# Kernel optimization log

Hardware: AMD Instinct MI355X
Metric: run time of the kernel (lower is better)

## Reference

```python
import jax, jax.numpy as jnp
import numpy as np

L_LANDMARKS = 64


def hyp_dist(x, y, c):
    """Faithful port of _compute_hyperbolic_distance for 3-D x,y.
    x:(B,N,D), y:(B,M,D) -> (B,N,M). Note: sqrt_c is computed but unused in the
    original, so only c enters via the `factor` term."""
    xn = jnp.sum(x * x, axis=-1)            # (B,N)
    yn = jnp.sum(y * y, axis=-1)            # (B,M)
    diff_sq = xn[:, :, None] + yn[:, None, :] - 2.0 * jnp.einsum('bnd,bmd->bnm', x, y)
    diff_sq = jnp.maximum(diff_sq, 1e-10)
    factor = (1.0 + c * xn)[:, :, None] + c * yn[:, None, :]
    return jnp.sqrt(diff_sq) * jnp.sqrt(jnp.maximum(factor, 1e-6))


def select_landmarks(emb, L, c):
    """MaxMin landmark selection. Original seeds with torch.randint; we use a
    deterministic seed index 0 per batch for reproducibility."""
    B, N, D = emb.shape
    first = jnp.zeros((B,), jnp.int32)

    def step(carry, _):
        min_d, prev = carry
        lm = jnp.take_along_axis(emb, prev[:, None, None].astype(jnp.int32), axis=1)  # (B,1,D)
        d = hyp_dist(emb, lm, c)[:, :, 0]        # (B,N)
        min_d = jnp.minimum(min_d, d)
        nxt = jnp.argmax(min_d, axis=1).astype(jnp.int32)
        return (min_d, nxt), nxt

    init = (jnp.full((B, N), jnp.inf, emb.dtype), first)
    _, rest = jax.lax.scan(step, init, None, length=L - 1)   # (L-1, B)
    idx = jnp.concatenate([first[None, :], rest], axis=0).T   # (B, L)
    landmarks = jnp.take_along_axis(emb, idx[:, :, None], axis=1)  # (B,L,D)
    return landmarks, idx


def witness_edge_weights(emb, landmarks, c):
    """Vectorized witness complex: for every point take its 2 nearest landmarks
    (i,j) and scatter-min the witness distance (dist to 2nd nearest) into the
    symmetric (L,L) edge weight matrix. Replaces the original B*N python loop."""
    B, N, D = emb.shape
    L = landmarks.shape[1]
    d = hyp_dist(emb, landmarks, c)              # (B,N,L)
    neg, idx2 = jax.lax.top_k(-d, 2)             # 2 smallest distances
    wd = -neg[..., 1]                            # witness distance (B,N)
    i = jnp.minimum(idx2[..., 0], idx2[..., 1])
    j = jnp.maximum(idx2[..., 0], idx2[..., 1])
    ew = jnp.full((B, L, L), jnp.inf, d.dtype)
    b = jnp.broadcast_to(jnp.arange(B)[:, None], (B, N))
    ew = ew.at[b, i, j].min(wd)
    ew = jnp.minimum(ew, jnp.swapaxes(ew, 1, 2))  # symmetrize
    return ew


def connected_components(adj):
    """Min-label propagation over the boolean adjacency; converges in <= L
    steps. labels[i] == min node index in i's component."""
    B, L, _ = adj.shape
    labels = jnp.broadcast_to(jnp.arange(L), (B, L))

    def body(_, labels):
        nb = jnp.min(jnp.where(adj, labels[:, None, :], L), axis=2)  # (B,L)
        return jnp.minimum(labels, nb)

    labels = jax.lax.fori_loop(0, L, body, labels)
    return jnp.sum(labels == jnp.arange(L), axis=1)  # number of components


def setup_inputs() -> dict:
    key = jax.random.key(0)
    k1, _ = jax.random.split(key)
    embeddings = jax.random.normal(k1, (8, 16384, 256), dtype=jnp.float32)
    curvature_scale = jnp.ones((), dtype=jnp.float32)
    return {"embeddings": embeddings, "curvature_scale": curvature_scale}


def reference(embeddings, curvature_scale):
    B, N, D = embeddings.shape
    L = min(L_LANDMARKS, N)
    c = jnp.abs(curvature_scale)
    landmarks, _ = select_landmarks(embeddings, L, c)
    ew = witness_edge_weights(embeddings, landmarks, c)
    adj = jnp.isfinite(ew)                       # (B,L,L), diag stays inf
    ncomp = connected_components(adj)            # (B,)
    n_edges = jnp.sum(jnp.triu(adj.astype(jnp.int32), 1), axis=(1, 2))
    # Kruskal-style counting: each redundant (cycle-closing) edge is a loop.
    beta_0 = ncomp.astype(jnp.float32)
    beta_1 = (n_edges - (L - ncomp)).astype(jnp.float32)
    fragmentation_score = beta_0 / L
    circular_reasoning = beta_1 > 3.0            # threshold_beta1 = 3
    return (beta_0, beta_1, fragmentation_score, circular_reasoning)
```

## Files before the change

### kernel.cpp

```cpp
#include <hip/hip_runtime.h>

static constexpr int B_ = 8;
static constexpr int N_ = 16384;
static constexpr int D_ = 256;
static constexpr int L_ = 64;

static constexpr int TPB = 512;
static constexpr int LF4 = 18;
static constexpr int RF4 = 64 - LF4;


__global__ void __launch_bounds__(1024)
init_kernel(unsigned int* __restrict__ z)
{
    z[blockIdx.x * 1024 + threadIdx.x] = 0u;
}

__global__ __attribute__((amdgpu_flat_work_group_size(512, 512),
                          amdgpu_waves_per_eu(2, 2)))
void fps_all_kernel(const float* __restrict__ emb, const float* __restrict__ csp,
                    unsigned long long* __restrict__ rec,
                    unsigned int* __restrict__ gadj,
                    unsigned int* __restrict__ cnt,
                    float* __restrict__ out)
{
    const int wg  = blockIdx.x;
    const int b   = wg & 7;
    const int wib = wg >> 3;
    const int tid = threadIdx.x;
    const int n   = (wib << 9) + tid;
    const float c = fabsf(csp[0]);

    __shared__ float4 slab[LF4 * TPB];
    __shared__ float wval[8];
    __shared__ int   widx[8];
    __shared__ float wxn[8];
    __shared__ int   s_next;
    __shared__ float s_lmn;
    __shared__ int   s_lead;
    __shared__ unsigned int lmask[128];
    __shared__ int   labels[64];

    if (tid < 128) lmask[tid] = 0u;

    const float4* __restrict__ pt = (const float4*)(emb + (size_t)(b * N_ + n) * D_);

    float4 p[RF4];
    float s0 = 0.f, s1 = 0.f, s2 = 0.f, s3 = 0.f;
    #pragma unroll
    for (int k = 0; k < LF4; ++k) {
        float4 v = pt[k];
        slab[k * TPB + tid] = v;
        s0 = fmaf(v.x, v.x, s0); s1 = fmaf(v.y, v.y, s1);
        s2 = fmaf(v.z, v.z, s2); s3 = fmaf(v.w, v.w, s3);
    }
    #pragma unroll
    for (int k = 0; k < RF4; ++k) {
        float4 v = pt[LF4 + k];
        p[k] = v;
        s0 = fmaf(v.x, v.x, s0); s1 = fmaf(v.y, v.y, s1);
        s2 = fmaf(v.z, v.z, s2); s3 = fmaf(v.w, v.w, s3);
    }
    const float my_xn = (s0 + s1) + (s2 + s3);

    float min_d = __builtin_inff();
    float b1v = __builtin_inff(), b2v = __builtin_inff();
    int   b1i = 0, b2i = 0;
    int   lm    = 0;
    float lmn_c = 0.f;

    #pragma unroll 1
    for (int s = 1; s <= L_; ++s) {
        const int lmU = __builtin_amdgcn_readfirstlane(lm);
        const float4* __restrict__ w4 =
            (const float4*)(emb + (size_t)(b * N_ + lmU) * D_);

        float lmn;
        if (s == 1) {
            float t0 = 0.f, t1 = 0.f, t2 = 0.f, t3 = 0.f;
            #pragma unroll
            for (int k = 0; k < 64; ++k) {
                float4 w = w4[k];
                t0 = fmaf(w.x, w.x, t0); t1 = fmaf(w.y, w.y, t1);
                t2 = fmaf(w.z, w.z, t2); t3 = fmaf(w.w, w.w, t3);
            }
            lmn = (t0 + t1) + (t2 + t3);
        } else {
            lmn = lmn_c;
        }

        float d0 = 0.f, d1 = 0.f, d2 = 0.f, d3 = 0.f;
        #pragma unroll
        for (int k = 0; k < LF4; ++k) {
            float4 v = slab[k * TPB + tid];
            float4 w = w4[k];
            d0 = fmaf(v.x, w.x, d0); d1 = fmaf(v.y, w.y, d1);
            d2 = fmaf(v.z, w.z, d2); d3 = fmaf(v.w, w.w, d3);
        }
        #pragma unroll
        for (int k = 0; k < RF4; ++k) {
            float4 v = p[k];
            float4 w = w4[LF4 + k];
            d0 = fmaf(v.x, w.x, d0); d1 = fmaf(v.y, w.y, d1);
            d2 = fmaf(v.z, w.z, d2); d3 = fmaf(v.w, w.w, d3);
        }
        const float dot  = (d0 + d1) + (d2 + d3);
        const float diff = fmaxf(my_xn + lmn - 2.f * dot, 1e-10f);
        const float fac  = fmaxf(1.f + c * my_xn + c * lmn, 1e-6f);
        const float d    = sqrtf(diff) * sqrtf(fac);

        if (d < b1v)      { b2v = b1v; b2i = b1i; b1v = d; b1i = s - 1; }
        else if (d < b2v) { b2v = d; b2i = s - 1; }

        if (s == L_) break;

        min_d = fminf(min_d, d);

        float v = min_d; int i = n; float x = my_xn;
        #pragma unroll
        for (int off = 32; off >= 1; off >>= 1) {
            float ov = __shfl_down(v, off);
            int   oi = __shfl_down(i, off);
            float ox = __shfl_down(x, off);
            if (ov > v || (ov == v && oi < i)) { v = ov; i = oi; x = ox; }
        }
        if ((tid & 63) == 0) {
            const int w = tid >> 6;
            wval[w] = v; widx[w] = i; wxn[w] = x;
        }
        __syncthreads();

        if (tid < 64) {
            v = (tid < 8) ? wval[tid] : -__builtin_inff();
            i = (tid < 8) ? widx[tid] : 0x7FFFFFFF;
            x = (tid < 8) ? wxn[tid]  : 0.f;
            #pragma unroll
            for (int off = 4; off >= 1; off >>= 1) {
                float ov = __shfl_down(v, off);
                int   oi = __shfl_down(i, off);
                float ox = __shfl_down(x, off);
                if (ov > v || (ov == v && oi < i)) { v = ov; i = oi; x = ox; }
            }
            const size_t sbase = (size_t)(b * 2 + (s & 1)) * 32 * 16;
            if (tid == 0) {
                const unsigned long long key =
                    ((unsigned long long)__float_as_uint(v) << 32) |
                    ((unsigned)(s & 0xFF) << 14) |
                    (unsigned)(16383 - i);
                const unsigned long long enc64 =
                    ((unsigned long long)(unsigned)s << 32) |
                    (unsigned long long)(unsigned)__float_as_uint(x);
                __hip_atomic_store(&rec[sbase + (size_t)wib * 16 + 0], key,
                                   __ATOMIC_RELAXED, __HIP_MEMORY_SCOPE_AGENT);
                __hip_atomic_store(&rec[sbase + (size_t)wib * 16 + 1], enc64,
                                   __ATOMIC_RELAXED, __HIP_MEMORY_SCOPE_AGENT);
            }
            unsigned long long myk, mye;
            for (;;) {
                myk = __hip_atomic_load(&rec[sbase + (size_t)(tid & 31) * 16 + 0],
                                        __ATOMIC_RELAXED, __HIP_MEMORY_SCOPE_AGENT);
                mye = __hip_atomic_load(&rec[sbase + (size_t)(tid & 31) * 16 + 1],
                                        __ATOMIC_RELAXED, __HIP_MEMORY_SCOPE_AGENT);
                const bool ok = (((myk >> 14) & 0xFFull) == (unsigned long long)(s & 0xFF)) &&
                                ((mye >> 32) == (unsigned long long)(unsigned)s);
                if (__all(ok)) break;
            }
            unsigned long long k = myk, e = mye;
            #pragma unroll
            for (int off = 32; off >= 1; off >>= 1) {
                unsigned long long ok2 = __shfl_down(k, off);
                unsigned long long oe  = __shfl_down(e, off);
                if (ok2 > k) { k = ok2; e = oe; }
            }
            if (tid == 0) {
                s_next = (int)(16383u - (unsigned)(k & 0x3FFFull));
                s_lmn  = __uint_as_float((unsigned)(e & 0xFFFFFFFFull));
            }
        }
        __syncthreads();
        lm    = s_next;
        lmn_c = s_lmn;
    }

    {
        const int lo = min(b1i, b2i), hi = max(b1i, b2i);
        const int bitpos = lo * 64 + hi;
        atomicOr(&lmask[bitpos >> 5], 1u << (bitpos & 31));
    }
    __syncthreads();
    if (tid < 128) {
        unsigned w = lmask[tid];
        if (w) atomicOr(&gadj[b * 128 + tid], w);
    }
    __syncthreads();

    if (tid == 0) {
        __threadfence();
        unsigned prev = atomicAdd(&cnt[b], 1u);
        s_lead = (prev == 31u) ? 1 : 0;
    }
    __syncthreads();
    if (!s_lead) return;

    __threadfence();
    if (tid < 128) lmask[tid] = atomicOr(&gadj[b * 128 + tid], 0u);
    __syncthreads();

    unsigned long long m = 0ull;
    if (tid < 64) {
        m = ((unsigned long long)lmask[tid * 2 + 1] << 32) | lmask[tid * 2];
        for (int j = 0; j < 64; ++j)
            if (lmask[j * 2 + (tid >> 5)] & (1u << (tid & 31))) m |= 1ull << j;
        labels[tid] = tid;
    }
    __syncthreads();

    for (int it = 0; it < 64; ++it) {
        int mn = 0;
        if (tid < 64) {
            mn = labels[tid];
            unsigned long long mm = m;
            while (mm) {
                int j = __ffsll(mm) - 1;
                int lj = labels[j];
                mn = mn < lj ? mn : lj;
                mm &= mm - 1;
            }
        }
        __syncthreads();
        if (tid < 64) labels[tid] = mn;
        __syncthreads();
    }

    if (tid < 64) {
        unsigned long long hi_mask = (tid < 63) ? (~0ull << (tid + 1)) : 0ull;
        int myedges = __popcll(m & hi_mask);
        int mycomp  = (labels[tid] == tid) ? 1 : 0;
        #pragma unroll
        for (int off = 32; off >= 1; off >>= 1) {
            myedges += __shfl_down(myedges, off);
            mycomp  += __shfl_down(mycomp, off);
        }
        if (tid == 0) {
            float beta0 = (float)mycomp;
            float beta1 = (float)(myedges - (64 - mycomp));
            out[b]      = beta0;
            out[8 + b]  = beta1;
            out[16 + b] = beta0 / 64.f;
            out[24 + b] = (beta1 > 3.f) ? 1.f : 0.f;
        }
    }
}

extern "C" void kernel_launch(void* const* d_in, const int* in_sizes, int n_in,
                              void* d_out, int out_size, void* d_ws, size_t ws_size,
                              hipStream_t stream)
{
    const float* emb = (const float*)d_in[0];
    const float* cs  = (const float*)d_in[1];
    float* out = (float*)d_out;

    char* ws = (char*)d_ws;
    unsigned long long* rec  = (unsigned long long*)(ws);
    unsigned int*       gadj = (unsigned int*)(ws + 65536);
    unsigned int*       cnt  = (unsigned int*)(ws + 69632);

    hipLaunchKernelGGL(init_kernel, dim3(18), dim3(1024), 0, stream,
                       (unsigned int*)ws);
    hipLaunchKernelGGL(fps_all_kernel, dim3(256), dim3(TPB), 0, stream,
                       emb, cs, rec, gadj, cnt, out);
}
```

Before: 554.2 us.

## Use leader-based reduce-and-broadcast for per-step cross-workgroup argmax

Replaces the all-to-all exchange, where each of the 32 workgroups per batch polled all 32 records, with a two-phase scheme. Records are packed contiguously. Workgroup 0 polls them, reduces to the global argmax and broadcasts the result into per-workgroup padded slots, and the other workgroups poll only their own slot. The goal is less polling traffic and cache-line contention on the global barrier. The cost is an extra serialized hop through the leader on every one of the 64 steps.

```diff
diff --git a/kernel.cpp b/kernel.cpp
--- a/kernel.cpp
+++ b/kernel.cpp
@@ -20,6 +20,7 @@
                           amdgpu_waves_per_eu(2, 2)))
 void fps_all_kernel(const float* __restrict__ emb, const float* __restrict__ csp,
                     unsigned long long* __restrict__ rec,
+                    unsigned long long* __restrict__ bcast,
                     unsigned int* __restrict__ gadj,
                     unsigned int* __restrict__ cnt,
                     float* __restrict__ out)
@@ -130,6 +131,12 @@
         }
         __syncthreads();
 
+        const int par = s & 1;
+        const size_t recbase = (size_t)(b * 2 + par) * 64;
+        const size_t bbase   = (size_t)(b * 2 + par) * 32 * 16;
+        const unsigned long long tagk = (unsigned long long)(s & 0xFF);
+        const unsigned long long tage = (unsigned long long)(unsigned)s;
+
         if (tid < 64) {
             v = (tid < 8) ? wval[tid] : -__builtin_inff();
             i = (tid < 8) ? widx[tid] : 0x7FFFFFFF;
@@ -141,7 +148,6 @@
                 float ox = __shfl_down(x, off);
                 if (ov > v || (ov == v && oi < i)) { v = ov; i = oi; x = ox; }
             }
-            const size_t sbase = (size_t)(b * 2 + (s & 1)) * 32 * 16;
             if (tid == 0) {
                 const unsigned long long key =
                     ((unsigned long long)__float_as_uint(v) << 32) |
@@ -150,31 +156,54 @@
                 const unsigned long long enc64 =
                     ((unsigned long long)(unsigned)s << 32) |
                     (unsigned long long)(unsigned)__float_as_uint(x);
-                __hip_atomic_store(&rec[sbase + (size_t)wib * 16 + 0], key,
+                __hip_atomic_store(&rec[recbase + (size_t)wib * 2 + 0], key,
                                    __ATOMIC_RELAXED, __HIP_MEMORY_SCOPE_AGENT);
-                __hip_atomic_store(&rec[sbase + (size_t)wib * 16 + 1], enc64,
+                __hip_atomic_store(&rec[recbase + (size_t)wib * 2 + 1], enc64,
                                    __ATOMIC_RELAXED, __HIP_MEMORY_SCOPE_AGENT);
             }
-            unsigned long long myk, mye;
-            for (;;) {
-                myk = __hip_atomic_load(&rec[sbase + (size_t)(tid & 31) * 16 + 0],
-                                        __ATOMIC_RELAXED, __HIP_MEMORY_SCOPE_AGENT);
-                mye = __hip_atomic_load(&rec[sbase + (size_t)(tid & 31) * 16 + 1],
-                                        __ATOMIC_RELAXED, __HIP_MEMORY_SCOPE_AGENT);
-                const bool ok = (((myk >> 14) & 0xFFull) == (unsigned long long)(s & 0xFF)) &&
-                                ((mye >> 32) == (unsigned long long)(unsigned)s);
-                if (__all(ok)) break;
-            }
-            unsigned long long k = myk, e = mye;
-            #pragma unroll
-            for (int off = 32; off >= 1; off >>= 1) {
-                unsigned long long ok2 = __shfl_down(k, off);
-                unsigned long long oe  = __shfl_down(e, off);
-                if (ok2 > k) { k = ok2; e = oe; }
-            }
-            if (tid == 0) {
-                s_next = (int)(16383u - (unsigned)(k & 0x3FFFull));
-                s_lmn  = __uint_as_float((unsigned)(e & 0xFFFFFFFFull));
+
+            if (wib == 0) {
+                unsigned long long myw;
+                for (;;) {
+                    myw = __hip_atomic_load(&rec[recbase + tid],
+                                            __ATOMIC_RELAXED, __HIP_MEMORY_SCOPE_AGENT);
+                    const bool ok = ((tid & 1) == 0)
+                        ? (((myw >> 14) & 0xFFull) == tagk)
+                        : ((myw >> 32) == tage);
+                    if (__all(ok)) break;
+                }
+                unsigned long long e = __shfl_down(myw, 1);
+                unsigned long long k = ((tid & 1) == 0) ? myw : 0ull;
+                #pragma unroll
+                for (int off = 32; off >= 2; off >>= 1) {
+                    unsigned long long ok2 = __shfl_down(k, off);
+                    unsigned long long oe  = __shfl_down(e, off);
+                    if (ok2 > k) { k = ok2; e = oe; }
+                }
+                const unsigned long long wk = __shfl(k, 0);
+                const unsigned long long we = __shfl(e, 0);
+                if (tid < 32) {
+                    __hip_atomic_store(&bcast[bbase + (size_t)tid * 16 + 0], wk,
+                                       __ATOMIC_RELAXED, __HIP_MEMORY_SCOPE_AGENT);
+                    __hip_atomic_store(&bcast[bbase + (size_t)tid * 16 + 1], we,
+                                       __ATOMIC_RELAXED, __HIP_MEMORY_SCOPE_AGENT);
+                }
+                if (tid == 0) {
+                    s_next = (int)(16383u - (unsigned)(wk & 0x3FFFull));
+                    s_lmn  = __uint_as_float((unsigned)(we & 0xFFFFFFFFull));
+                }
+            } else if (tid == 0) {
+                unsigned long long bk, be;
+                for (;;) {
+                    bk = __hip_atomic_load(&bcast[bbase + (size_t)wib * 16 + 0],
+                                           __ATOMIC_RELAXED, __HIP_MEMORY_SCOPE_AGENT);
+                    be = __hip_atomic_load(&bcast[bbase + (size_t)wib * 16 + 1],
+                                           __ATOMIC_RELAXED, __HIP_MEMORY_SCOPE_AGENT);
+                    if ((((bk >> 14) & 0xFFull) == tagk) && ((be >> 32) == tage))
+                        break;
+                }
+                s_next = (int)(16383u - (unsigned)(bk & 0x3FFFull));
+                s_lmn  = __uint_as_float((unsigned)(be & 0xFFFFFFFFull));
             }
         }
         __syncthreads();
@@ -261,12 +290,13 @@
     float* out = (float*)d_out;
 
     char* ws = (char*)d_ws;
-    unsigned long long* rec  = (unsigned long long*)(ws);
-    unsigned int*       gadj = (unsigned int*)(ws + 65536);
-    unsigned int*       cnt  = (unsigned int*)(ws + 69632);
-
-    hipLaunchKernelGGL(init_kernel, dim3(18), dim3(1024), 0, stream,
+    unsigned long long* rec   = (unsigned long long*)(ws);
+    unsigned long long* bcast = (unsigned long long*)(ws + 8192);
+    unsigned int*       gadj  = (unsigned int*)(ws + 73728);
+    unsigned int*       cnt   = (unsigned int*)(ws + 77824);
+
+    hipLaunchKernelGGL(init_kernel, dim3(20), dim3(1024), 0, stream,
                        (unsigned int*)ws);
     hipLaunchKernelGGL(fps_all_kernel, dim3(256), dim3(TPB), 0, stream,
-                       emb, cs, rec, gadj, cnt, out);
+                       emb, cs, rec, bcast, gadj, cnt, out);
 }
```

Result: no change. 551.0 us (-0.6%).
